# Performance work log

Hardware: AMD Instinct MI355X
Metric: run time of the kernel (lower is better)

## Reference

```python
import jax, jax.numpy as jnp
import numpy as np

AVG_NOBJ = 49.0
NEG_SLOPE = 0.01  # torch leaky_relu default


def eops_1_to_2(x, nobj, aggregation):
    """x: [B,N,C] -> [B,C,5,N,N] equivariant basis (rank-1 -> rank-2)."""
    B, N, C = x.shape
    xt = jnp.transpose(x, (0, 2, 1))  # B,C,N
    if aggregation == 'sum':
        agg = xt.sum(-1) / AVG_NOBJ                      # B,C
    elif aggregation == 'mean':
        agg = xt.sum(-1) / nobj[:, None]                 # B,C
    elif aggregation == 'max':
        agg = xt.max(-1)
    elif aggregation == 'min':
        agg = xt.min(-1)
    eye = jnp.eye(N, dtype=x.dtype)                      # N,N
    op1 = xt[:, :, :, None] * eye                        # x_i on diagonal
    op2 = jnp.broadcast_to(xt[:, :, None, :], (B, C, N, N))  # x_j along rows
    op3 = jnp.broadcast_to(xt[:, :, :, None], (B, C, N, N))  # x_i along cols
    op4 = agg[:, :, None, None] * eye                    # agg on diagonal
    op5 = jnp.broadcast_to(agg[:, :, None, None], (B, C, N, N))  # agg everywhere
    return jnp.stack([op1, op2, op3, op4, op5], axis=2)  # B,C,5,N,N


def setup_inputs() -> dict:
    key = jax.random.key(0)
    k1, k2 = jax.random.split(key)
    B, N, C, S = 8, 128, 64, 64
    basis_total = 5 * 4  # 5 basis ops per config char, config='smxn'
    inputs = jax.random.normal(k1, (B, N, C), dtype=jnp.float32)
    mask = jnp.ones((B, N, N, 1), dtype=jnp.float32)
    nobj = jnp.full((B,), 100.0, dtype=jnp.float32)
    coefs = jax.random.normal(k2, (C, S, basis_total), dtype=jnp.float32) * np.sqrt(2.0 / (C * basis_total)).astype(np.float32)
    bias = jnp.zeros((S,), dtype=jnp.float32)
    return {"inputs": inputs, "mask": mask, "nobj": nobj, "coefs": coefs, "bias": bias}


def reference(inputs, mask, nobj, coefs, bias):
    # config = 'smxn' -> sum, mean, max, min basis tensors, concat on basis axis
    ops = jnp.concatenate(
        [eops_1_to_2(inputs, nobj, a) for a in ('sum', 'mean', 'max', 'min')],
        axis=2)  # B,C,20,N,N
    out = jnp.einsum('dsb,ndbij->nijs', coefs, ops)      # B,N,N,S
    out = out + bias[None, None, None, :]
    out = jnp.where(out >= 0, out, NEG_SLOPE * out)      # leaky_relu
    return out * mask
```

## Files before the change

### kernel.cpp

```cpp
#include <hip/hip_runtime.h>

constexpr int B = 8, N = 128, C = 64, S = 64;
constexpr float INV_AVG = 1.0f / 49.0f;
constexpr float SLOPE = 0.01f;

typedef float f4 __attribute__((ext_vector_type(4)));

constexpr int WS_A  = 0;
constexpr int WS_R  = 65536;
constexpr int WS_C  = 131072;
constexpr int WS_D  = 196608;
constexpr int WS_E  = 197120;
constexpr int WS_W1 = 197632;
constexpr int WS_W2 = 201728;
constexpr int WS_W3 = 205824;

__global__ __launch_bounds__(256) void weights_agg_kernel(
    const float* __restrict__ x,
    const float* __restrict__ nobj,
    const float* __restrict__ coefs,
    float* __restrict__ ws)
{
  const int tid = threadIdx.x;
  if (blockIdx.x < 16) {
    const int e = blockIdx.x * 256 + tid;
    const float4* cp = (const float4*)(coefs + e * 20);
    float4 f0 = cp[0], f1 = cp[1], f2 = cp[2], f3 = cp[3], f4v = cp[4];
    ws[WS_W1 + e] = f0.x + f1.y + f2.z + f3.w;
    ws[WS_W2 + e] = f0.y + f1.z + f2.w + f4v.x;
    ws[WS_W3 + e] = f0.z + f1.w + f3.x + f4v.y;
  } else {
    __shared__ float smem[9216];
    const int n = blockIdx.x - 16;
    float* xs  = smem;
    float* ps  = smem + 8192;
    __shared__ float pmx[256], pmn[256], ag[256];

    const float4* xg = (const float4*)(x + n * N * C);
    float4* xs4 = (float4*)xs;
#pragma unroll
    for (int k = 0; k < 8; ++k) xs4[tid + k * 256] = xg[tid + k * 256];
    __syncthreads();

    const int d = tid & 63, grp = tid >> 6;
    float sm = 0.f, mx = -INFINITY, mn = INFINITY;
    for (int i = grp * 32; i < grp * 32 + 32; ++i) {
      float v = xs[i * 64 + d];
      sm += v;
      mx = fmaxf(mx, v);
      mn = fminf(mn, v);
    }
    ps [grp * 64 + d] = sm;
    pmx[grp * 64 + d] = mx;
    pmn[grp * 64 + d] = mn;
    __syncthreads();

    if (tid < 64) {
      float s0 = ps[tid] + ps[64 + tid] + ps[128 + tid] + ps[192 + tid];
      float m0 = fmaxf(fmaxf(pmx[tid], pmx[64 + tid]),
                       fmaxf(pmx[128 + tid], pmx[192 + tid]));
      float n0 = fminf(fminf(pmn[tid], pmn[64 + tid]),
                       fminf(pmn[128 + tid], pmn[192 + tid]));
      ag[tid]       = s0 * INV_AVG;
      ag[64 + tid]  = s0 / nobj[n];
      ag[128 + tid] = m0;
      ag[192 + tid] = n0;
    }
    __syncthreads();

    if (tid < 64) {
      const int s = tid;
      float dv = 0.f, ev = 0.f;
      for (int d2 = 0; d2 < 64; ++d2) {
        const float* cp = coefs + d2 * (S * 20) + s * 20;
        float a0 = ag[d2], a1 = ag[64 + d2], a2 = ag[128 + d2], a3 = ag[192 + d2];
        dv += a0 * cp[3] + a1 * cp[8] + a2 * cp[13] + a3 * cp[18];
        ev += a0 * cp[4] + a1 * cp[9] + a2 * cp[14] + a3 * cp[19];
      }
      ws[WS_D + n * S + s] = dv;
      ws[WS_E + n * S + s] = ev;
    }
  }
}

__global__ __launch_bounds__(256) void gemm_kernel(
    const float* __restrict__ x,
    const float* __restrict__ ws_r,
    float* __restrict__ ws)
{
  __shared__ float xs[16 * 64];
  const int n  = blockIdx.x >> 3;
  const int i0 = (blockIdx.x & 7) << 4;
  const int tid = threadIdx.x;

  ((float4*)xs)[tid] = ((const float4*)(x + (n * N + i0) * C))[tid];
  __syncthreads();

  const int s = tid & 63;
  const int g = tid >> 6;
  const float* W1 = ws_r + WS_W1;
  const float* W2 = ws_r + WS_W2;
  const float* W3 = ws_r + WS_W3;

  float a1[4] = {0,0,0,0}, a2[4] = {0,0,0,0}, a3[4] = {0,0,0,0};
#pragma unroll 8
  for (int d = 0; d < 64; ++d) {
    float w1 = W1[d * 64 + s];
    float w2 = W2[d * 64 + s];
    float w3 = W3[d * 64 + s];
#pragma unroll
    for (int k = 0; k < 4; ++k) {
      float xv = xs[(g * 4 + k) * 64 + d];
      a1[k] += xv * w1;
      a2[k] += xv * w2;
      a3[k] += xv * w3;
    }
  }
#pragma unroll
  for (int k = 0; k < 4; ++k) {
    const int o = (n * N + i0 + g * 4 + k) * S + s;
    ws[WS_A + o] = a1[k];
    ws[WS_R + o] = a2[k];
    ws[WS_C + o] = a3[k];
  }
}

__global__ __launch_bounds__(256) void assemble_kernel(
    const float* __restrict__ ws,
    const float* __restrict__ mask,
    const float* __restrict__ bias,
    float* __restrict__ out)
{
  const int bi = blockIdx.x;
  const int n  = bi >> 7;
  const int i  = bi & 127;
  const int l  = threadIdx.x & 15;
  const int jg = threadIdx.x >> 4;

  const float4* A4 = (const float4*)(ws + WS_A);
  const float4* R4 = (const float4*)(ws + WS_R);
  const float4* C4 = (const float4*)(ws + WS_C);
  const float4* D4 = (const float4*)(ws + WS_D);
  const float4* E4 = (const float4*)(ws + WS_E);

  float4 cc = C4[bi * 16 + l];
  float4 ee = E4[n * 16 + l];
  float4 bb = ((const float4*)bias)[l];
  float bx = cc.x + ee.x + bb.x;
  float by = cc.y + ee.y + bb.y;
  float bz = cc.z + ee.z + bb.z;
  float bw = cc.w + ee.w + bb.w;

  f4* out4 = (f4*)out + (size_t)bi * (N * 16);

#pragma unroll
  for (int t = 0; t < 8; ++t) {
    const int j = jg + t * 16;
    float4 rr = R4[(n * N + j) * 16 + l];
    float  m  = mask[bi * N + j];
    float v0 = bx + rr.x;
    float v1 = by + rr.y;
    float v2 = bz + rr.z;
    float v3 = bw + rr.w;
    if (j == i) {
      float4 aa = A4[bi * 16 + l];
      float4 dd = D4[n * 16 + l];
      v0 += aa.x + dd.x; v1 += aa.y + dd.y;
      v2 += aa.z + dd.z; v3 += aa.w + dd.w;
    }
    v0 = (v0 >= 0.f) ? v0 : SLOPE * v0;
    v1 = (v1 >= 0.f) ? v1 : SLOPE * v1;
    v2 = (v2 >= 0.f) ? v2 : SLOPE * v2;
    v3 = (v3 >= 0.f) ? v3 : SLOPE * v3;
    f4 o;
    o.x = v0 * m; o.y = v1 * m; o.z = v2 * m; o.w = v3 * m;
    __builtin_nontemporal_store(o, &out4[j * 16 + l]);
  }
}

extern "C" void kernel_launch(void* const* d_in, const int* in_sizes, int n_in,
                              void* d_out, int out_size, void* d_ws, size_t ws_size,
                              hipStream_t stream) {
  const float* x     = (const float*)d_in[0];
  const float* mask  = (const float*)d_in[1];
  const float* nobj  = (const float*)d_in[2];
  const float* coefs = (const float*)d_in[3];
  const float* bias  = (const float*)d_in[4];
  float* out = (float*)d_out;
  float* ws  = (float*)d_ws;

  weights_agg_kernel<<<24, 256, 0, stream>>>(x, nobj, coefs, ws);
  gemm_kernel<<<64, 256, 0, stream>>>(x, ws, ws);
  assemble_kernel<<<1024, 256, 0, stream>>>(ws, mask, bias, out);
}
```

Measured before the change: 89.50 us.

## Fuse weight folding and projection GEMM into one prep kernel

Merges the weight-folding, aggregation and projection GEMM kernels into a single launch. Each GEMM block now folds the full coefficient tensor into shared memory itself, and aggregation blocks run alongside. This removes one kernel launch and the global round trip for the folded weights. The cost is that every one of the 64 GEMM blocks redundantly reads the whole 320KB coefs tensor and uses about 52KB of LDS.

```diff
diff --git a/kernel.cpp b/kernel.cpp
--- a/kernel.cpp
+++ b/kernel.cpp
@@ -11,30 +11,66 @@
 constexpr int WS_C  = 131072;
 constexpr int WS_D  = 196608;
 constexpr int WS_E  = 197120;
-constexpr int WS_W1 = 197632;
-constexpr int WS_W2 = 201728;
-constexpr int WS_W3 = 205824;
 
-__global__ __launch_bounds__(256) void weights_agg_kernel(
+__global__ __launch_bounds__(256) void prep_kernel(
     const float* __restrict__ x,
     const float* __restrict__ nobj,
     const float* __restrict__ coefs,
     float* __restrict__ ws)
 {
+  __shared__ float smem[13312];
   const int tid = threadIdx.x;
-  if (blockIdx.x < 16) {
-    const int e = blockIdx.x * 256 + tid;
-    const float4* cp = (const float4*)(coefs + e * 20);
-    float4 f0 = cp[0], f1 = cp[1], f2 = cp[2], f3 = cp[3], f4v = cp[4];
-    ws[WS_W1 + e] = f0.x + f1.y + f2.z + f3.w;
-    ws[WS_W2 + e] = f0.y + f1.z + f2.w + f4v.x;
-    ws[WS_W3 + e] = f0.z + f1.w + f3.x + f4v.y;
+
+  if (blockIdx.x < 64) {
+    float* W1 = smem;
+    float* W2 = smem + 4096;
+    float* W3 = smem + 8192;
+    float* xs = smem + 12288;
+    const int n  = blockIdx.x >> 3;
+    const int i0 = (blockIdx.x & 7) << 4;
+
+#pragma unroll
+    for (int k = 0; k < 16; ++k) {
+      const int e = k * 256 + tid;
+      const float4* cp = (const float4*)(coefs + e * 20);
+      float4 f0 = cp[0], f1 = cp[1], f2 = cp[2], f3 = cp[3], f4v = cp[4];
+      W1[e] = f0.x + f1.y + f2.z + f3.w;
+      W2[e] = f0.y + f1.z + f2.w + f4v.x;
+      W3[e] = f0.z + f1.w + f3.x + f4v.y;
+    }
+    ((float4*)xs)[tid] = ((const float4*)(x + (n * N + i0) * C))[tid];
+    __syncthreads();
+
+    const int s = tid & 63;
+    const int g = tid >> 6;
+    float a1[4] = {0,0,0,0}, a2[4] = {0,0,0,0}, a3[4] = {0,0,0,0};
+#pragma unroll 8
+    for (int d = 0; d < 64; ++d) {
+      float w1 = W1[d * 64 + s];
+      float w2 = W2[d * 64 + s];
+      float w3 = W3[d * 64 + s];
+#pragma unroll
+      for (int k = 0; k < 4; ++k) {
+        float xv = xs[(g * 4 + k) * 64 + d];
+        a1[k] += xv * w1;
+        a2[k] += xv * w2;
+        a3[k] += xv * w3;
+      }
+    }
+#pragma unroll
+    for (int k = 0; k < 4; ++k) {
+      const int o = (n * N + i0 + g * 4 + k) * S + s;
+      ws[WS_A + o] = a1[k];
+      ws[WS_R + o] = a2[k];
+      ws[WS_C + o] = a3[k];
+    }
   } else {
-    __shared__ float smem[9216];
-    const int n = blockIdx.x - 16;
+    const int n = blockIdx.x - 64;
     float* xs  = smem;
     float* ps  = smem + 8192;
-    __shared__ float pmx[256], pmn[256], ag[256];
+    float* pmx = smem + 8448;
+    float* pmn = smem + 8704;
+    float* ag  = smem + 8960;
 
     const float4* xg = (const float4*)(x + n * N * C);
     float4* xs4 = (float4*)xs;
@@ -80,48 +116,6 @@
       ws[WS_D + n * S + s] = dv;
       ws[WS_E + n * S + s] = ev;
     }
-  }
-}
-
-__global__ __launch_bounds__(256) void gemm_kernel(
-    const float* __restrict__ x,
-    const float* __restrict__ ws_r,
-    float* __restrict__ ws)
-{
-  __shared__ float xs[16 * 64];
-  const int n  = blockIdx.x >> 3;
-  const int i0 = (blockIdx.x & 7) << 4;
-  const int tid = threadIdx.x;
-
-  ((float4*)xs)[tid] = ((const float4*)(x + (n * N + i0) * C))[tid];
-  __syncthreads();
-
-  const int s = tid & 63;
-  const int g = tid >> 6;
-  const float* W1 = ws_r + WS_W1;
-  const float* W2 = ws_r + WS_W2;
-  const float* W3 = ws_r + WS_W3;
-
-  float a1[4] = {0,0,0,0}, a2[4] = {0,0,0,0}, a3[4] = {0,0,0,0};
-#pragma unroll 8
-  for (int d = 0; d < 64; ++d) {
-    float w1 = W1[d * 64 + s];
-    float w2 = W2[d * 64 + s];
-    float w3 = W3[d * 64 + s];
-#pragma unroll
-    for (int k = 0; k < 4; ++k) {
-      float xv = xs[(g * 4 + k) * 64 + d];
-      a1[k] += xv * w1;
-      a2[k] += xv * w2;
-      a3[k] += xv * w3;
-    }
-  }
-#pragma unroll
-  for (int k = 0; k < 4; ++k) {
-    const int o = (n * N + i0 + g * 4 + k) * S + s;
-    ws[WS_A + o] = a1[k];
-    ws[WS_R + o] = a2[k];
-    ws[WS_C + o] = a3[k];
   }
 }
 
@@ -189,7 +183,6 @@
   float* out = (float*)d_out;
   float* ws  = (float*)d_ws;
 
-  weights_agg_kernel<<<24, 256, 0, stream>>>(x, nobj, coefs, ws);
-  gemm_kernel<<<64, 256, 0, stream>>>(x, ws, ws);
+  prep_kernel<<<72, 256, 0, stream>>>(x, nobj, coefs, ws);
   assemble_kernel<<<1024, 256, 0, stream>>>(ws, mask, bias, out);
 }
```

After: 83.13 us. 1.08x faster.
